# Kernel tuning notes

Measured on AMD Instinct MI355X. Metric: run time of the kernel, lower is better.

Reference implementation:

```python
import jax, jax.numpy as jnp
import numpy as np

PRESERVE_RATIO = 0.8
TEMPERATURE = 1.5


def setup_inputs() -> dict:
    key = jax.random.key(0)
    ks = jax.random.split(key, 8)
    B, C, H, W = 2, 64, 96, 96
    inter = C // 2
    bott = C // 4
    s = 0.02
    return {
        "x": jax.random.normal(ks[0], (B, C, H, W), dtype=jnp.float32),
        "g_w": jax.random.normal(ks[1], (inter, C), dtype=jnp.float32) * s,
        "theta_w": jax.random.normal(ks[2], (inter, C), dtype=jnp.float32) * s,
        "phi_w": jax.random.normal(ks[3], (inter, C), dtype=jnp.float32) * s,
        "W_w": jax.random.normal(ks[4], (C, inter), dtype=jnp.float32) * s,
        "cg1_w": jax.random.normal(ks[5], (bott, C), dtype=jnp.float32) * s,
        "cg1_b": jnp.zeros((bott,), dtype=jnp.float32),
        "cg2_w": jax.random.normal(ks[6], (C, bott), dtype=jnp.float32) * s,
        "cg2_b": jnp.zeros((C,), dtype=jnp.float32),
    }


def reference(x, g_w, theta_w, phi_w, W_w, cg1_w, cg1_b, cg2_w, cg2_b):
    B, C, H, W = x.shape
    N = H * W
    # color gate: global avg pool -> 1x1 conv -> relu -> 1x1 conv -> sigmoid
    pooled = jnp.mean(x, axis=(2, 3))                       # [B, C]
    h = jax.nn.relu(pooled @ cg1_w.T + cg1_b)               # [B, C//4]
    gate = jax.nn.sigmoid(h @ cg2_w.T + cg2_b)              # [B, C]

    xf = x.reshape(B, C, N)                                 # [B, C, N]
    g_x = jnp.einsum('ic,bcn->bni', g_w, xf)                # [B, N, I]
    theta = jnp.einsum('ic,bcn->bni', theta_w, xf)          # [B, N, I]
    phi = jnp.einsum('ic,bcn->bin', phi_w, xf)              # [B, I, N]

    affinity = jnp.einsum('bni,bim->bnm', theta, phi) / TEMPERATURE  # [B, N, N]
    affinity = jax.nn.softmax(affinity, axis=-1)
    y = jnp.einsum('bnm,bmi->bni', affinity, g_x)           # [B, N, I]
    y = jnp.einsum('ci,bni->bcn', W_w, y).reshape(B, C, H, W)
    y = y * gate[:, :, None, None] * PRESERVE_RATIO
    return x + y
```

## Files before the change

kernel.cpp:

```cpp
#include <hip/hip_runtime.h>

#define N_TOK 9216
#define C_DIM 64
#define I_DIM 32
#define BOT 16
#define B_SZ 2
#define N_TILES 144

typedef short bf16x8 __attribute__((ext_vector_type(8)));
typedef float f32x4 __attribute__((ext_vector_type(4)));
typedef float f32x16 __attribute__((ext_vector_type(16)));

__device__ __forceinline__ unsigned packbf(float a, float b) {
  return __builtin_amdgcn_perm(__float_as_uint(b), __float_as_uint(a), 0x07060302u);
}
__device__ __forceinline__ unsigned short bftrunc(float f) {
  return (unsigned short)(__float_as_uint(f) >> 16);
}
__device__ __forceinline__ float bflo(unsigned u) {
  return __uint_as_float(u << 16);
}
__device__ __forceinline__ float bfhi(unsigned u) {
  return __uint_as_float(u & 0xffff0000u);
}

__global__ __launch_bounds__(256) void proj_pool_kernel(
    const float* __restrict__ x, const float* __restrict__ g_w,
    const float* __restrict__ theta_w, const float* __restrict__ phi_w,
    unsigned short* __restrict__ Q, unsigned short* __restrict__ K,
    unsigned short* __restrict__ VT, float* __restrict__ pooled) {
  if (blockIdx.x >= 864) {
    int bc = blockIdx.x - 864;
    const float* p = x + (size_t)bc * N_TOK;
    float s = 0.f;
    for (int t = threadIdx.x; t < N_TOK; t += 256) s += p[t];
#pragma unroll
    for (int off = 32; off >= 1; off >>= 1) s += __shfl_down(s, off, 64);
    __shared__ float red[4];
    int wid = threadIdx.x >> 6, lane = threadIdx.x & 63;
    if (lane == 0) red[wid] = s;
    __syncthreads();
    if (threadIdx.x == 0)
      pooled[bc] = (red[0] + red[1] + red[2] + red[3]) * (1.0f / N_TOK);
    return;
  }
  const int lane = threadIdx.x & 63;
  const int m = lane & 15, quad = lane >> 4;
  int task = blockIdx.x * 4 + (threadIdx.x >> 6);
  int mat = task / 1152;
  int r0 = task % 1152;
  int b = r0 / 576;
  int n0 = (r0 % 576) * 16;
  const float* wsrc = (mat == 0) ? theta_w : ((mat == 1) ? phi_w : g_w);
  const float scale = (mat == 0) ? 0.96179669439f : 1.0f;

  bf16x8 afr[2][2];
#pragma unroll
  for (int it = 0; it < 2; ++it)
#pragma unroll
    for (int cs = 0; cs < 2; ++cs) {
      const float* wp = wsrc + (it * 16 + m) * C_DIM + cs * 32 + quad * 8;
      union { unsigned u[4]; bf16x8 v; } t;
#pragma unroll
      for (int j = 0; j < 4; ++j)
        t.u[j] = packbf(wp[2 * j] * scale, wp[2 * j + 1] * scale);
      afr[it][cs] = t.v;
    }

  const float* xb = x + (size_t)b * C_DIM * N_TOK + n0 + m;
  bf16x8 bfr[2];
#pragma unroll
  for (int cs = 0; cs < 2; ++cs) {
    union { unsigned u[4]; bf16x8 v; } t;
#pragma unroll
    for (int j = 0; j < 4; ++j) {
      float v0 = xb[(size_t)(cs * 32 + quad * 8 + 2 * j) * N_TOK];
      float v1 = xb[(size_t)(cs * 32 + quad * 8 + 2 * j + 1) * N_TOK];
      t.u[j] = packbf(v0, v1);
    }
    bfr[cs] = t.v;
  }

  f32x4 acc[2] = {{0.f, 0.f, 0.f, 0.f}, {0.f, 0.f, 0.f, 0.f}};
#pragma unroll
  for (int cs = 0; cs < 2; ++cs)
#pragma unroll
    for (int it = 0; it < 2; ++it)
      acc[it] = __builtin_amdgcn_mfma_f32_16x16x32_bf16(afr[it][cs], bfr[cs],
                                                        acc[it], 0, 0, 0);
  if (mat < 2) {
    unsigned short* dst =
        ((mat == 0) ? Q : K) + ((size_t)b * N_TOK + n0 + m) * I_DIM;
#pragma unroll
    for (int it = 0; it < 2; ++it) {
      unsigned u0 = packbf(acc[it][0], acc[it][1]);
      unsigned u1 = packbf(acc[it][2], acc[it][3]);
      *(uint2*)(dst + it * 16 + quad * 4) = make_uint2(u0, u1);
    }
  } else {
#pragma unroll
    for (int it = 0; it < 2; ++it)
#pragma unroll
      for (int r = 0; r < 4; ++r)
        VT[((size_t)b * I_DIM + it * 16 + quad * 4 + r) * N_TOK + n0 + m] =
            bftrunc(acc[it][r]);
  }
}

__device__ __forceinline__ void tilework(const f32x16 s, const bf16x8 bvA,
                                         const bf16x8 bvB, f32x16& accy,
                                         float& lsum) {
  float e[16];
#pragma unroll
  for (int r = 0; r < 16; ++r) e[r] = __builtin_amdgcn_exp2f(s[r]);
  float l0 = 0.f, l1 = 0.f, l2 = 0.f, l3 = 0.f;
#pragma unroll
  for (int r = 0; r < 4; ++r) {
    l0 += e[r]; l1 += e[4 + r]; l2 += e[8 + r]; l3 += e[12 + r];
  }
  lsum += (l0 + l1) + (l2 + l3);
  unsigned pk[8];
#pragma unroll
  for (int i = 0; i < 8; ++i) pk[i] = packbf(e[2 * i], e[2 * i + 1]);
  asm("v_permlane32_swap_b32 %0, %1" : "+v"(pk[0]), "+v"(pk[2]));
  asm("v_permlane32_swap_b32 %0, %1" : "+v"(pk[1]), "+v"(pk[3]));
  asm("v_permlane32_swap_b32 %0, %1" : "+v"(pk[4]), "+v"(pk[6]));
  asm("v_permlane32_swap_b32 %0, %1" : "+v"(pk[5]), "+v"(pk[7]));
  union { unsigned u[4]; bf16x8 v; } A0, A1;
  A0.u[0] = pk[0]; A0.u[1] = pk[1]; A0.u[2] = pk[2]; A0.u[3] = pk[3];
  A1.u[0] = pk[4]; A1.u[1] = pk[5]; A1.u[2] = pk[6]; A1.u[3] = pk[7];
  accy = __builtin_amdgcn_mfma_f32_32x32x16_bf16(A0.v, bvA, accy, 0, 0, 0);
  accy = __builtin_amdgcn_mfma_f32_32x32x16_bf16(A1.v, bvB, accy, 0, 0, 0);
}

__device__ __forceinline__ void loadK(bf16x8 a[4], const unsigned short* kp) {
  a[0] = *(const bf16x8*)(kp);
  a[1] = *(const bf16x8*)(kp + 16);
  a[2] = *(const bf16x8*)(kp + 32 * I_DIM);
  a[3] = *(const bf16x8*)(kp + 32 * I_DIM + 16);
}

__global__ __launch_bounds__(256, 4) void attn_kernel(
    const unsigned short* __restrict__ Q, const unsigned short* __restrict__ Kg,
    const unsigned short* __restrict__ VT, unsigned short* __restrict__ Ypart,
    float* __restrict__ Lpart, int tps) {
  const int lane = threadIdx.x & 63;
  const int l32 = lane & 31, h = lane >> 5;
  const int qw = blockIdx.x * 4 + (threadIdx.x >> 6);
  const int ks = blockIdx.y, b = blockIdx.z;
  const int q0 = qw * 32;
  const unsigned short* Qb = Q + (size_t)b * N_TOK * I_DIM;
  const unsigned short* Kb = Kg + (size_t)b * N_TOK * I_DIM;
  const unsigned short* Vb = VT + (size_t)b * I_DIM * N_TOK;

  bf16x8 bq0 = *(const bf16x8*)(Qb + (size_t)(q0 + l32) * I_DIM + h * 8);
  bf16x8 bq1 = *(const bf16x8*)(Qb + (size_t)(q0 + l32) * I_DIM + 16 + h * 8);

  f32x16 accy = {};
  float lsum = 0.f;

  const int kt0 = ks * tps;
  const unsigned short* kp = Kb + ((size_t)kt0 * 64 + l32) * I_DIM + h * 8;
  const unsigned short* vp0 = Vb + (size_t)l32 * N_TOK + kt0 * 64 + h * 8;

  const f32x16 zz = {};
  bf16x8 ak[4];
  loadK(ak, kp);
  for (int kt = 0; kt < tps; ++kt) {
    kp += 64 * I_DIM;
    bf16x8 nak[4];
    loadK(nak, kp);
    const unsigned short* vp = vp0 + kt * 64;
    bf16x8 bv0 = *(const bf16x8*)(vp);
    bf16x8 bv1 = *(const bf16x8*)(vp + 16);
    bf16x8 bv2 = *(const bf16x8*)(vp + 32);
    bf16x8 bv3 = *(const bf16x8*)(vp + 48);

    f32x16 s0 = __builtin_amdgcn_mfma_f32_32x32x16_bf16(ak[0], bq0, zz, 0, 0, 0);
    s0 = __builtin_amdgcn_mfma_f32_32x32x16_bf16(ak[1], bq1, s0, 0, 0, 0);
    f32x16 s1 = __builtin_amdgcn_mfma_f32_32x32x16_bf16(ak[2], bq0, zz, 0, 0, 0);
    s1 = __builtin_amdgcn_mfma_f32_32x32x16_bf16(ak[3], bq1, s1, 0, 0, 0);

    tilework(s0, bv0, bv1, accy, lsum);
    tilework(s1, bv2, bv3, accy, lsum);

    ak[0] = nak[0]; ak[1] = nak[1]; ak[2] = nak[2]; ak[3] = nak[3];
  }

  lsum += __shfl_xor(lsum, 32, 64);

  const size_t base = (size_t)(ks * B_SZ + b) * N_TOK + q0;
#pragma unroll
  for (int R = 0; R < 4; ++R)
#pragma unroll
    for (int r = 0; r < 4; ++r)
      Ypart[(base + r + 8 * R + 4 * h) * I_DIM + l32] = bftrunc(accy[4 * R + r]);
  if (h == 0) Lpart[base + l32] = lsum;
}

__global__ __launch_bounds__(256) void epilogue_kernel(
    const float* __restrict__ x, const float* __restrict__ W_w,
    const float* __restrict__ pooled, const float* __restrict__ cg1_w,
    const float* __restrict__ cg1_b, const float* __restrict__ cg2_w,
    const float* __restrict__ cg2_b, const unsigned short* __restrict__ Ypart,
    const float* __restrict__ Lpart, float* __restrict__ out, int KS) {
  __shared__ float Ysh[64][33];
  __shared__ float lsh[64];
  __shared__ float gsh[64];
  __shared__ float hl[BOT];
  const int t = threadIdx.x;
  const int b = blockIdx.y;
  const int n0 = blockIdx.x * 64;

  if (t < BOT) {
    float a = cg1_b[t];
#pragma unroll
    for (int c = 0; c < C_DIM; ++c)
      a += cg1_w[t * C_DIM + c] * pooled[b * C_DIM + c];
    hl[t] = a > 0.f ? a : 0.f;
  }

  {
    int nl = t >> 2, i0 = (t & 3) * 8;
    float s[8];
#pragma unroll
    for (int k = 0; k < 8; ++k) s[k] = 0.f;
    for (int ks = 0; ks < KS; ++ks) {
      const unsigned short* yp =
          Ypart + ((size_t)(ks * B_SZ + b) * N_TOK + n0 + nl) * I_DIM + i0;
      uint4 v = *(const uint4*)yp;
      s[0] += bflo(v.x); s[1] += bfhi(v.x);
      s[2] += bflo(v.y); s[3] += bfhi(v.y);
      s[4] += bflo(v.z); s[5] += bfhi(v.z);
      s[6] += bflo(v.w); s[7] += bfhi(v.w);
    }
#pragma unroll
    for (int k = 0; k < 8; ++k) Ysh[nl][i0 + k] = s[k];
    if (t < 64) {
      float ls = 0.f;
      for (int ks = 0; ks < KS; ++ks)
        ls += Lpart[(size_t)(ks * B_SZ + b) * N_TOK + n0 + t];
      lsh[t] = ls;
    }
  }
  __syncthreads();

  if (t < C_DIM) {
    float z = cg2_b[t];
#pragma unroll
    for (int j = 0; j < BOT; ++j) z += cg2_w[t * BOT + j] * hl[j];
    gsh[t] = 0.8f / (1.f + __expf(-z));
  }
  __syncthreads();

  const int n = t & 63, cg = t >> 6;
  float y[I_DIM];
#pragma unroll
  for (int i = 0; i < I_DIM; ++i) y[i] = Ysh[n][i];
  const float inv = 1.0f / lsh[n];
  const float* xb = x + ((size_t)b * C_DIM + cg * 16) * N_TOK + n0 + n;
  float* ob = out + ((size_t)b * C_DIM + cg * 16) * N_TOK + n0 + n;
#pragma unroll
  for (int c16 = 0; c16 < 16; ++c16) {
    const int c = cg * 16 + c16;
    float sacc = 0.f;
#pragma unroll
    for (int i = 0; i < I_DIM; ++i) sacc += W_w[c * I_DIM + i] * y[i];
    ob[(size_t)c16 * N_TOK] = xb[(size_t)c16 * N_TOK] + gsh[c] * inv * sacc;
  }
}

extern "C" void kernel_launch(void* const* d_in, const int* in_sizes, int n_in,
                              void* d_out, int out_size, void* d_ws, size_t ws_size,
                              hipStream_t stream) {
  const float* x = (const float*)d_in[0];
  const float* g_w = (const float*)d_in[1];
  const float* theta_w = (const float*)d_in[2];
  const float* phi_w = (const float*)d_in[3];
  const float* W_w = (const float*)d_in[4];
  const float* cg1_w = (const float*)d_in[5];
  const float* cg1_b = (const float*)d_in[6];
  const float* cg2_w = (const float*)d_in[7];
  const float* cg2_b = (const float*)d_in[8];
  float* out = (float*)d_out;

  char* w = (char*)d_ws;
  const size_t bfsz = (size_t)B_SZ * N_TOK * I_DIM * sizeof(unsigned short);
  unsigned short* Qb = (unsigned short*)(w);
  unsigned short* Kb = (unsigned short*)(w + bfsz);
  unsigned short* VT = (unsigned short*)(w + 2 * bfsz);
  float* pooled = (float*)(w + 3 * bfsz);
  char* w2 = w + 3 * bfsz + 8192;

  int KS = 16;
  {
    const size_t per = (size_t)B_SZ * N_TOK * (I_DIM * 2 + 4);
    while (KS > 1 && (3 * bfsz + 8192 + (size_t)KS * per) > ws_size) KS >>= 1;
  }
  float* Lpart = (float*)w2;
  unsigned short* Ypart =
      (unsigned short*)(w2 + (size_t)KS * B_SZ * N_TOK * sizeof(float));
  int tps = N_TILES / KS;

  proj_pool_kernel<<<dim3(992), 256, 0, stream>>>(x, g_w, theta_w, phi_w, Qb,
                                                  Kb, VT, pooled);
  attn_kernel<<<dim3(72, KS, B_SZ), 256, 0, stream>>>(Qb, Kb, VT, Ypart, Lpart, tps);
  epilogue_kernel<<<dim3(N_TOK / 64, B_SZ), 256, 0, stream>>>(
      x, W_w, pooled, cg1_w, cg1_b, cg2_w, cg2_b, Ypart, Lpart, out, KS);
}
```

Measured before the change: 175.4 us.

## Stage K/V tiles in shared LDS across waves and batch projection tokens

```diff
diff --git a/kernel.cpp b/kernel.cpp
--- a/kernel.cpp
+++ b/kernel.cpp
@@ -11,6 +11,9 @@
 typedef float f32x4 __attribute__((ext_vector_type(4)));
 typedef float f32x16 __attribute__((ext_vector_type(16)));
 
+#define KST 36
+#define VST 68
+
 __device__ __forceinline__ unsigned packbf(float a, float b) {
   return __builtin_amdgcn_perm(__float_as_uint(b), __float_as_uint(a), 0x07060302u);
 }
@@ -29,8 +32,8 @@
     const float* __restrict__ theta_w, const float* __restrict__ phi_w,
     unsigned short* __restrict__ Q, unsigned short* __restrict__ K,
     unsigned short* __restrict__ VT, float* __restrict__ pooled) {
-  if (blockIdx.x >= 864) {
-    int bc = blockIdx.x - 864;
+  if (blockIdx.x >= 216) {
+    int bc = blockIdx.x - 216;
     const float* p = x + (size_t)bc * N_TOK;
     float s = 0.f;
     for (int t = threadIdx.x; t < N_TOK; t += 256) s += p[t];
@@ -47,10 +50,10 @@
   const int lane = threadIdx.x & 63;
   const int m = lane & 15, quad = lane >> 4;
   int task = blockIdx.x * 4 + (threadIdx.x >> 6);
-  int mat = task / 1152;
-  int r0 = task % 1152;
-  int b = r0 / 576;
-  int n0 = (r0 % 576) * 16;
+  int mat = task / 288;
+  int r0 = task % 288;
+  int b = r0 / 144;
+  int n0 = (r0 % 144) * 64;
   const float* wsrc = (mat == 0) ? theta_w : ((mat == 1) ? phi_w : g_w);
   const float scale = (mat == 0) ? 0.96179669439f : 1.0f;
 
@@ -67,43 +70,47 @@
       afr[it][cs] = t.v;
     }
 
-  const float* xb = x + (size_t)b * C_DIM * N_TOK + n0 + m;
-  bf16x8 bfr[2];
-#pragma unroll
-  for (int cs = 0; cs < 2; ++cs) {
-    union { unsigned u[4]; bf16x8 v; } t;
-#pragma unroll
-    for (int j = 0; j < 4; ++j) {
-      float v0 = xb[(size_t)(cs * 32 + quad * 8 + 2 * j) * N_TOK];
-      float v1 = xb[(size_t)(cs * 32 + quad * 8 + 2 * j + 1) * N_TOK];
-      t.u[j] = packbf(v0, v1);
-    }
-    bfr[cs] = t.v;
-  }
-
-  f32x4 acc[2] = {{0.f, 0.f, 0.f, 0.f}, {0.f, 0.f, 0.f, 0.f}};
-#pragma unroll
-  for (int cs = 0; cs < 2; ++cs)
-#pragma unroll
-    for (int it = 0; it < 2; ++it)
-      acc[it] = __builtin_amdgcn_mfma_f32_16x16x32_bf16(afr[it][cs], bfr[cs],
-                                                        acc[it], 0, 0, 0);
-  if (mat < 2) {
-    unsigned short* dst =
-        ((mat == 0) ? Q : K) + ((size_t)b * N_TOK + n0 + m) * I_DIM;
-#pragma unroll
-    for (int it = 0; it < 2; ++it) {
-      unsigned u0 = packbf(acc[it][0], acc[it][1]);
-      unsigned u1 = packbf(acc[it][2], acc[it][3]);
-      *(uint2*)(dst + it * 16 + quad * 4) = make_uint2(u0, u1);
-    }
-  } else {
-#pragma unroll
-    for (int it = 0; it < 2; ++it)
-#pragma unroll
-      for (int r = 0; r < 4; ++r)
-        VT[((size_t)b * I_DIM + it * 16 + quad * 4 + r) * N_TOK + n0 + m] =
-            bftrunc(acc[it][r]);
+#pragma unroll
+  for (int sub = 0; sub < 4; ++sub) {
+    const int ns = n0 + sub * 16;
+    const float* xb = x + (size_t)b * C_DIM * N_TOK + ns + m;
+    bf16x8 bfr[2];
+#pragma unroll
+    for (int cs = 0; cs < 2; ++cs) {
+      union { unsigned u[4]; bf16x8 v; } t;
+#pragma unroll
+      for (int j = 0; j < 4; ++j) {
+        float v0 = xb[(size_t)(cs * 32 + quad * 8 + 2 * j) * N_TOK];
+        float v1 = xb[(size_t)(cs * 32 + quad * 8 + 2 * j + 1) * N_TOK];
+        t.u[j] = packbf(v0, v1);
+      }
+      bfr[cs] = t.v;
+    }
+
+    f32x4 acc[2] = {{0.f, 0.f, 0.f, 0.f}, {0.f, 0.f, 0.f, 0.f}};
+#pragma unroll
+    for (int cs = 0; cs < 2; ++cs)
+#pragma unroll
+      for (int it = 0; it < 2; ++it)
+        acc[it] = __builtin_amdgcn_mfma_f32_16x16x32_bf16(afr[it][cs], bfr[cs],
+                                                          acc[it], 0, 0, 0);
+    if (mat < 2) {
+      unsigned short* dst =
+          ((mat == 0) ? Q : K) + ((size_t)b * N_TOK + ns + m) * I_DIM;
+#pragma unroll
+      for (int it = 0; it < 2; ++it) {
+        unsigned u0 = packbf(acc[it][0], acc[it][1]);
+        unsigned u1 = packbf(acc[it][2], acc[it][3]);
+        *(uint2*)(dst + it * 16 + quad * 4) = make_uint2(u0, u1);
+      }
+    } else {
+#pragma unroll
+      for (int it = 0; it < 2; ++it)
+#pragma unroll
+        for (int r = 0; r < 4; ++r)
+          VT[((size_t)b * I_DIM + it * 16 + quad * 4 + r) * N_TOK + ns + m] =
+              bftrunc(acc[it][r]);
+    }
   }
 }
 
@@ -133,58 +140,87 @@
   accy = __builtin_amdgcn_mfma_f32_32x32x16_bf16(A1.v, bvB, accy, 0, 0, 0);
 }
 
-__device__ __forceinline__ void loadK(bf16x8 a[4], const unsigned short* kp) {
-  a[0] = *(const bf16x8*)(kp);
-  a[1] = *(const bf16x8*)(kp + 16);
-  a[2] = *(const bf16x8*)(kp + 32 * I_DIM);
-  a[3] = *(const bf16x8*)(kp + 32 * I_DIM + 16);
+__device__ __forceinline__ bf16x8 lds_frag(const unsigned short* p) {
+  union { uint2 d[2]; bf16x8 v; } t;
+  t.d[0] = *(const uint2*)(p);
+  t.d[1] = *(const uint2*)(p + 4);
+  return t.v;
 }
 
 __global__ __launch_bounds__(256, 4) void attn_kernel(
     const unsigned short* __restrict__ Q, const unsigned short* __restrict__ Kg,
     const unsigned short* __restrict__ VT, unsigned short* __restrict__ Ypart,
     float* __restrict__ Lpart, int tps) {
-  const int lane = threadIdx.x & 63;
+  const int tid = threadIdx.x;
+  const int lane = tid & 63;
   const int l32 = lane & 31, h = lane >> 5;
-  const int qw = blockIdx.x * 4 + (threadIdx.x >> 6);
   const int ks = blockIdx.y, b = blockIdx.z;
-  const int q0 = qw * 32;
+  const int q0 = blockIdx.x * 128 + (tid >> 6) * 32;
   const unsigned short* Qb = Q + (size_t)b * N_TOK * I_DIM;
   const unsigned short* Kb = Kg + (size_t)b * N_TOK * I_DIM;
   const unsigned short* Vb = VT + (size_t)b * I_DIM * N_TOK;
 
+  __shared__ __align__(16) unsigned short Ks[64 * KST];
+  __shared__ __align__(16) unsigned short Vs[32 * VST];
+
   bf16x8 bq0 = *(const bf16x8*)(Qb + (size_t)(q0 + l32) * I_DIM + h * 8);
   bf16x8 bq1 = *(const bf16x8*)(Qb + (size_t)(q0 + l32) * I_DIM + 16 + h * 8);
 
   f32x16 accy = {};
   float lsum = 0.f;
+  const f32x16 zz = {};
 
   const int kt0 = ks * tps;
-  const unsigned short* kp = Kb + ((size_t)kt0 * 64 + l32) * I_DIM + h * 8;
-  const unsigned short* vp0 = Vb + (size_t)l32 * N_TOK + kt0 * 64 + h * 8;
-
-  const f32x16 zz = {};
-  bf16x8 ak[4];
-  loadK(ak, kp);
+  const int kr = tid >> 2, kc = (tid & 3) * 8;
+  const int vr = tid >> 3, vc = (tid & 7) * 8;
+  const unsigned short* kgp = Kb + ((size_t)kt0 * 64 + kr) * I_DIM + kc;
+  const unsigned short* vgp = Vb + (size_t)vr * N_TOK + kt0 * 64 + vc;
+  unsigned short* klp = &Ks[kr * KST + kc];
+  unsigned short* vlp = &Vs[vr * VST + vc];
+
+  {
+    uint4 rk = *(const uint4*)kgp;
+    uint4 rv = *(const uint4*)vgp;
+    *(uint2*)(klp) = make_uint2(rk.x, rk.y);
+    *(uint2*)(klp + 4) = make_uint2(rk.z, rk.w);
+    *(uint2*)(vlp) = make_uint2(rv.x, rv.y);
+    *(uint2*)(vlp + 4) = make_uint2(rv.z, rv.w);
+  }
+
   for (int kt = 0; kt < tps; ++kt) {
-    kp += 64 * I_DIM;
-    bf16x8 nak[4];
-    loadK(nak, kp);
-    const unsigned short* vp = vp0 + kt * 64;
-    bf16x8 bv0 = *(const bf16x8*)(vp);
-    bf16x8 bv1 = *(const bf16x8*)(vp + 16);
-    bf16x8 bv2 = *(const bf16x8*)(vp + 32);
-    bf16x8 bv3 = *(const bf16x8*)(vp + 48);
-
-    f32x16 s0 = __builtin_amdgcn_mfma_f32_32x32x16_bf16(ak[0], bq0, zz, 0, 0, 0);
-    s0 = __builtin_amdgcn_mfma_f32_32x32x16_bf16(ak[1], bq1, s0, 0, 0, 0);
-    f32x16 s1 = __builtin_amdgcn_mfma_f32_32x32x16_bf16(ak[2], bq0, zz, 0, 0, 0);
-    s1 = __builtin_amdgcn_mfma_f32_32x32x16_bf16(ak[3], bq1, s1, 0, 0, 0);
+    __syncthreads();
+    const bool pf = (kt + 1 < tps);
+    uint4 rk = {0, 0, 0, 0}, rv = {0, 0, 0, 0};
+    if (pf) {
+      rk = *(const uint4*)(kgp + (size_t)(kt + 1) * 64 * I_DIM);
+      rv = *(const uint4*)(vgp + (kt + 1) * 64);
+    }
+    asm volatile("" ::: "memory");
+
+    bf16x8 ak00 = lds_frag(&Ks[l32 * KST + 8 * h]);
+    bf16x8 ak01 = lds_frag(&Ks[l32 * KST + 16 + 8 * h]);
+    bf16x8 ak10 = lds_frag(&Ks[(32 + l32) * KST + 8 * h]);
+    bf16x8 ak11 = lds_frag(&Ks[(32 + l32) * KST + 16 + 8 * h]);
+    bf16x8 bv0 = lds_frag(&Vs[l32 * VST + 8 * h]);
+    bf16x8 bv1 = lds_frag(&Vs[l32 * VST + 16 + 8 * h]);
+    bf16x8 bv2 = lds_frag(&Vs[l32 * VST + 32 + 8 * h]);
+    bf16x8 bv3 = lds_frag(&Vs[l32 * VST + 48 + 8 * h]);
+
+    f32x16 s0 = __builtin_amdgcn_mfma_f32_32x32x16_bf16(ak00, bq0, zz, 0, 0, 0);
+    s0 = __builtin_amdgcn_mfma_f32_32x32x16_bf16(ak01, bq1, s0, 0, 0, 0);
+    f32x16 s1 = __builtin_amdgcn_mfma_f32_32x32x16_bf16(ak10, bq0, zz, 0, 0, 0);
+    s1 = __builtin_amdgcn_mfma_f32_32x32x16_bf16(ak11, bq1, s1, 0, 0, 0);
 
     tilework(s0, bv0, bv1, accy, lsum);
     tilework(s1, bv2, bv3, accy, lsum);
 
-    ak[0] = nak[0]; ak[1] = nak[1]; ak[2] = nak[2]; ak[3] = nak[3];
+    __syncthreads();
+    if (pf) {
+      *(uint2*)(klp) = make_uint2(rk.x, rk.y);
+      *(uint2*)(klp + 4) = make_uint2(rk.z, rk.w);
+      *(uint2*)(vlp) = make_uint2(rv.x, rv.y);
+      *(uint2*)(vlp + 4) = make_uint2(rv.z, rv.w);
+    }
   }
 
   lsum += __shfl_xor(lsum, 32, 64);
@@ -302,7 +338,7 @@
       (unsigned short*)(w2 + (size_t)KS * B_SZ * N_TOK * sizeof(float));
   int tps = N_TILES / KS;
 
-  proj_pool_kernel<<<dim3(992), 256, 0, stream>>>(x, g_w, theta_w, phi_w, Qb,
+  proj_pool_kernel<<<dim3(344), 256, 0, stream>>>(x, g_w, theta_w, phi_w, Qb,
                                                   Kb, VT, pooled);
   attn_kernel<<<dim3(72, KS, B_SZ), 256, 0, stream>>>(Qb, Kb, VT, Ypart, Lpart, tps);
   epilogue_kernel<<<dim3(N_TOK / 64, B_SZ), 256, 0, stream>>>(
```

New measurement: 142.2 us. -18.9%, faster.
